# Performance work log

Hardware: AMD Instinct MI355X
Metric: run time of the kernel (lower is better)

## Reference

```python
import jax, jax.numpy as jnp
import numpy as np

B, S, D = 4, 2048, 2048


def setup_inputs() -> dict:
    key = jax.random.key(0)
    ks = jax.random.split(key, 24)
    sc = 1.0 / np.sqrt(D)
    def lin(ki, kb):
        W = jax.random.normal(ks[ki], (D, D), dtype=jnp.float32) * sc
        b = jax.random.normal(ks[kb], (D,), dtype=jnp.float32) * 0.01
        return W, b
    Wi, bWi = lin(0, 1); Ui, bUi = lin(2, 3)
    Wf, bWf = lin(4, 5); Uf, bUf = lin(6, 7)
    Wc, bWc = lin(8, 9); Uc, bUc = lin(10, 11)
    Wo, bWo = lin(12, 13); Uo, bUo = lin(14, 15)
    Wp, bp = lin(16, 17)
    x = jax.random.normal(ks[18], (B, S, D), dtype=jnp.float32)
    h = jax.random.normal(ks[19], (B, S, D), dtype=jnp.float32)
    return dict(x=x, h=h, Wi=Wi, bWi=bWi, Ui=Ui, bUi=bUi,
                Wf=Wf, bWf=bWf, Uf=Uf, bUf=bUf,
                Wc=Wc, bWc=bWc, Uc=Uc, bUc=bUc,
                Wo=Wo, bWo=bWo, Uo=Uo, bUo=bUo,
                Wp=Wp, bp=bp)


def reference(x, h, Wi, bWi, Ui, bUi, Wf, bWf, Uf, bUf,
              Wc, bWc, Uc, bUc, Wo, bWo, Uo, bUo, Wp, bp):
    # In the torch source, h[:, t, :] is read BEFORE being overwritten at step t,
    # and c is zero-initialized with each slot written once (so f * c_prev == 0).
    # Hence the computation is exactly parallel over the time axis.
    Zi = jnp.einsum('bsd,ed->bse', x, Wi) + bWi + jnp.einsum('bsd,ed->bse', h, Ui) + bUi
    Zf = jnp.einsum('bsd,ed->bse', x, Wf) + bWf + jnp.einsum('bsd,ed->bse', h, Uf) + bUf
    Zc = jnp.einsum('bsd,ed->bse', x, Wc) + bWc + jnp.einsum('bsd,ed->bse', h, Uc) + bUc
    Zo = jnp.einsum('bsd,ed->bse', x, Wo) + bWo + jnp.einsum('bsd,ed->bse', h, Uo) + bUo
    i = jnp.exp(Zi)
    f = jnp.exp(Zf)  # multiplies a zero cell state in the source; kept for fidelity
    c = f * jnp.zeros_like(f) + i * jnp.tanh(Zc)
    h_out = jax.nn.sigmoid(Zo) * jnp.tanh(c)
    hidden_state = h_out[:, -1, :] @ Wp.T + bp
    return (hidden_state, c)
```

## Files before the change

kernel.cpp:

```cpp
#include <hip/hip_runtime.h>
#include <hip/hip_bf16.h>

typedef short short8 __attribute__((ext_vector_type(8)));
typedef unsigned short ushort8v __attribute__((ext_vector_type(8)));
typedef float f32x4 __attribute__((ext_vector_type(4)));

#define D_DIM 2048
#define KTOT 4096
#define M_TOT 8192
#define NPACK 4096


__device__ __forceinline__ unsigned short f2bf(float f) {
    union { float f; unsigned u; } c; c.f = f;
    unsigned u = c.u;
    u += 0x7fffu + ((u >> 16) & 1u);
    return (unsigned short)(u >> 16);
}

__device__ __forceinline__ float fast_tanh(float x) {
    float ax = fabsf(x);
    float ez = __expf(2.0f * fminf(ax, 15.0f));
    float t = (ez - 1.0f) / (ez + 1.0f);
    return copysignf(t, x);
}

#define GLOAD_LDS16(g, l)                                                     \
    __builtin_amdgcn_global_load_lds(                                         \
        (const __attribute__((address_space(1))) void*)(g),                   \
        (__attribute__((address_space(3))) void*)(l), 16, 0, 0)


__global__ __launch_bounds__(256)
void pack2(const float* __restrict__ X, const float* __restrict__ H,
           __hip_bfloat16* __restrict__ dst, int total8) {
    int t = blockIdx.x * 256 + threadIdx.x;
    if (t >= total8) return;
    long e0 = (long)t * 8;
    long r  = e0 >> 12;
    int  k  = (int)(e0 & 4095);
    const float* src = (k < D_DIM) ? (X + r * D_DIM + k)
                                   : (H + r * D_DIM + (k - D_DIM));
    float4 v0 = *(const float4*)(src);
    float4 v1 = *(const float4*)(src + 4);
    ushort8v o;
    o[0] = f2bf(v0.x); o[1] = f2bf(v0.y); o[2] = f2bf(v0.z); o[3] = f2bf(v0.w);
    o[4] = f2bf(v1.x); o[5] = f2bf(v1.y); o[6] = f2bf(v1.z); o[7] = f2bf(v1.w);
    *(ushort8v*)(dst + e0) = o;
}


__global__ __launch_bounds__(256)
void pack_gates(const float* __restrict__ Wi, const float* __restrict__ Ui,
                const float* __restrict__ Wc, const float* __restrict__ Uc,
                __hip_bfloat16* __restrict__ dst) {
    int t = blockIdx.x * 256 + threadIdx.x;
    const int g = t >> 9;
    const int k = (t & 511) * 8;
    const int w = g & 31;
    const int n = ((g >> 5) << 4) | (w & 15);
    const float* Wm = (w & 16) ? Wc : Wi;
    const float* Um = (w & 16) ? Uc : Ui;
    const float* src = (k < D_DIM) ? (Wm + (size_t)n * D_DIM + k)
                                   : (Um + (size_t)n * D_DIM + (k - D_DIM));
    float4 v0 = *(const float4*)(src);
    float4 v1 = *(const float4*)(src + 4);
    ushort8v o;
    o[0] = f2bf(v0.x); o[1] = f2bf(v0.y); o[2] = f2bf(v0.z); o[3] = f2bf(v0.w);
    o[4] = f2bf(v1.x); o[5] = f2bf(v1.y); o[6] = f2bf(v1.z); o[7] = f2bf(v1.w);
    *(ushort8v*)(dst + (size_t)g * KTOT + k) = o;
}


#define BK 64
#define NT (KTOT / BK)

__device__ __forceinline__ void stage_half(const __hip_bfloat16* __restrict__ mat,
                                           __hip_bfloat16* ldsHalf,
                                           int rowbase, int kcol0,
                                           int wid, int lane) {
    #pragma unroll
    for (int j = 0; j < 2; ++j) {
        const int Lb  = wid * 128 + j * 64;
        const int L   = Lb + lane;
        const int row = L >> 2;
        const int ul  = (L & 3) ^ ((L >> 3) & 3);
        const __hip_bfloat16* src =
            mat + (size_t)(rowbase + row) * KTOT + kcol0 + ul * 8;
        GLOAD_LDS16(src, (char*)ldsHalf + Lb * 16);
    }
}

__global__ __launch_bounds__(512, 2)
void gemm8(const __hip_bfloat16* __restrict__ A,
           const __hip_bfloat16* __restrict__ Bp,
           const float* __restrict__ bWi, const float* __restrict__ bUi,
           const float* __restrict__ bWc, const float* __restrict__ bUc,
           float* __restrict__ Cout) {
    __shared__ __hip_bfloat16 sA[2][2][256][32];
    __shared__ __hip_bfloat16 sB[2][2][256][32];

    const int tid  = threadIdx.x;
    const int wid  = tid >> 6;
    const int lane = tid & 63;

    int bid = blockIdx.x;
    bid = (bid & 7) * 64 + (bid >> 3);
    const int tn = (bid & 15) * 256;
    const int tm = (bid >> 4) * 256;

    const int wr  = (wid >> 2) * 128;
    const int wc  = (wid & 3) * 64;
    const int r15 = lane & 15;
    const int uswz16 = (((lane >> 4) ^ ((r15 >> 1) & 3)) * 16);

    f32x4 acc[8][4] = {};

    stage_half(A,  &sA[0][0][0][0], tm, 0,  wid, lane);
    stage_half(Bp, &sB[0][0][0][0], tn, 0,  wid, lane);
    stage_half(A,  &sA[0][1][0][0], tm, 32, wid, lane);
    stage_half(Bp, &sB[0][1][0][0], tn, 32, wid, lane);
    asm volatile("s_waitcnt vmcnt(4)" ::: "memory");
    __builtin_amdgcn_s_barrier();

    short8 af[4], bf[4];

    for (int t = 0; t < NT; ++t) {
        const int cur = t & 1, nxt = cur ^ 1;
        const bool pf = (t + 1 < NT);
        const int kc1 = (t + 1) * BK;
        const char* pA = (const char*)sA[cur];
        const char* pB = (const char*)sB[cur];

        #pragma unroll
        for (int m = 0; m < 4; ++m)
            af[m] = *(const short8*)(pA + (size_t)(wr + m * 16 + r15) * 64 + uswz16);
        #pragma unroll
        for (int n = 0; n < 4; ++n)
            bf[n] = *(const short8*)(pB + (size_t)(wc + n * 16 + r15) * 64 + uswz16);
        if (pf) stage_half(A, &sA[nxt][0][0][0], tm, kc1, wid, lane);
        __builtin_amdgcn_s_barrier();
        asm volatile("s_waitcnt lgkmcnt(0)" ::: "memory");
        __builtin_amdgcn_s_setprio(1);
        #pragma unroll
        for (int m = 0; m < 4; ++m)
            #pragma unroll
            for (int n = 0; n < 4; ++n)
                acc[m][n] = __builtin_amdgcn_mfma_f32_16x16x32_bf16(
                    af[m], bf[n], acc[m][n], 0, 0, 0);
        __builtin_amdgcn_s_setprio(0);
        __builtin_amdgcn_s_barrier();

        #pragma unroll
        for (int m = 0; m < 4; ++m)
            af[m] = *(const short8*)(pA + (size_t)(wr + 64 + m * 16 + r15) * 64 + uswz16);
        if (pf) stage_half(Bp, &sB[nxt][0][0][0], tn, kc1, wid, lane);
        __builtin_amdgcn_s_barrier();
        asm volatile("s_waitcnt lgkmcnt(0)" ::: "memory");
        __builtin_amdgcn_s_setprio(1);
        #pragma unroll
        for (int m = 0; m < 4; ++m)
            #pragma unroll
            for (int n = 0; n < 4; ++n)
                acc[4 + m][n] = __builtin_amdgcn_mfma_f32_16x16x32_bf16(
                    af[m], bf[n], acc[4 + m][n], 0, 0, 0);
        __builtin_amdgcn_s_setprio(0);
        if (t < NT - 1) asm volatile("s_waitcnt vmcnt(4)" ::: "memory");
        else            asm volatile("s_waitcnt vmcnt(0)" ::: "memory");
        __builtin_amdgcn_s_barrier();

        #pragma unroll
        for (int m = 0; m < 4; ++m)
            af[m] = *(const short8*)(pA + 16384 + (size_t)(wr + m * 16 + r15) * 64 + uswz16);
        #pragma unroll
        for (int n = 0; n < 4; ++n)
            bf[n] = *(const short8*)(pB + 16384 + (size_t)(wc + n * 16 + r15) * 64 + uswz16);
        if (pf) stage_half(A, &sA[nxt][1][0][0], tm, kc1 + 32, wid, lane);
        __builtin_amdgcn_s_barrier();
        asm volatile("s_waitcnt lgkmcnt(0)" ::: "memory");
        __builtin_amdgcn_s_setprio(1);
        #pragma unroll
        for (int m = 0; m < 4; ++m)
            #pragma unroll
            for (int n = 0; n < 4; ++n)
                acc[m][n] = __builtin_amdgcn_mfma_f32_16x16x32_bf16(
                    af[m], bf[n], acc[m][n], 0, 0, 0);
        __builtin_amdgcn_s_setprio(0);
        __builtin_amdgcn_s_barrier();

        #pragma unroll
        for (int m = 0; m < 4; ++m)
            af[m] = *(const short8*)(pA + 16384 + (size_t)(wr + 64 + m * 16 + r15) * 64 + uswz16);
        if (pf) stage_half(Bp, &sB[nxt][1][0][0], tn, kc1 + 32, wid, lane);
        __builtin_amdgcn_s_barrier();
        asm volatile("s_waitcnt lgkmcnt(0)" ::: "memory");
        __builtin_amdgcn_s_setprio(1);
        #pragma unroll
        for (int m = 0; m < 4; ++m)
            #pragma unroll
            for (int n = 0; n < 4; ++n)
                acc[4 + m][n] = __builtin_amdgcn_mfma_f32_16x16x32_bf16(
                    af[m], bf[n], acc[4 + m][n], 0, 0, 0);
        __builtin_amdgcn_s_setprio(0);
        asm volatile("s_waitcnt vmcnt(4)" ::: "memory");
        __builtin_amdgcn_s_barrier();
    }

    const int rg4 = (lane >> 4) * 4;
    #pragma unroll
    for (int q = 0; q < 2; ++q) {
        const int gn = (tn >> 1) + (wc >> 1) + q * 16 + r15;
        const float bi_ = bWi[gn] + bUi[gn];
        const float bc_ = bWc[gn] + bUc[gn];
        #pragma unroll
        for (int m = 0; m < 8; ++m) {
            const int gm = tm + wr + m * 16 + rg4;
            #pragma unroll
            for (int r = 0; r < 4; ++r) {
                const float zi = acc[m][2 * q][r]     + bi_;
                const float zc = acc[m][2 * q + 1][r] + bc_;
                Cout[(size_t)(gm + r) * D_DIM + gn] = __expf(zi) * fast_tanh(zc);
            }
        }
    }
}


__global__ __launch_bounds__(256)
void last_gate(const float* __restrict__ x, const float* __restrict__ h,
               const float* __restrict__ Wo, const float* __restrict__ bWo,
               const float* __restrict__ Uo, const float* __restrict__ bUo,
               const float* __restrict__ cfull, float* __restrict__ hbuf) {
    const int o    = blockIdx.x * 4 + (threadIdx.x >> 6);
    const int lane = threadIdx.x & 63;
    const int b = o >> 11, e = o & 2047;
    const float* xr = x  + ((size_t)b * D_DIM + (D_DIM - 1)) * D_DIM;
    const float* hr = h  + ((size_t)b * D_DIM + (D_DIM - 1)) * D_DIM;
    const float* wo = Wo + (size_t)e * D_DIM;
    const float* uo = Uo + (size_t)e * D_DIM;
    float s = 0.0f;
    for (int d = lane; d < D_DIM; d += 64)
        s += xr[d] * wo[d] + hr[d] * uo[d];
    #pragma unroll
    for (int off = 32; off; off >>= 1) s += __shfl_down(s, off);
    if (lane == 0) {
        const float zo  = s + bWo[e] + bUo[e];
        const float sig = 1.0f / (1.0f + __expf(-zo));
        const float cv  = cfull[((size_t)b * D_DIM + (D_DIM - 1)) * D_DIM + e];
        hbuf[o] = sig * fast_tanh(cv);
    }
}


__global__ __launch_bounds__(256)
void proj(const float* __restrict__ hbuf, const float* __restrict__ Wp,
          const float* __restrict__ bp, float* __restrict__ out) {
    const int o    = blockIdx.x * 4 + (threadIdx.x >> 6);
    const int lane = threadIdx.x & 63;
    const int b = o >> 11, p = o & 2047;
    const float* hv = hbuf + (size_t)b * D_DIM;
    const float* wp = Wp   + (size_t)p * D_DIM;
    float s = 0.0f;
    for (int e = lane; e < D_DIM; e += 64)
        s += hv[e] * wp[e];
    #pragma unroll
    for (int off = 32; off; off >>= 1) s += __shfl_down(s, off);
    if (lane == 0) out[o] = s + bp[p];
}


extern "C" void kernel_launch(void* const* d_in, const int* in_sizes, int n_in,
                              void* d_out, int out_size, void* d_ws, size_t ws_size,
                              hipStream_t stream) {
    const float* x   = (const float*)d_in[0];
    const float* h   = (const float*)d_in[1];
    const float* Wi  = (const float*)d_in[2];  const float* bWi = (const float*)d_in[3];
    const float* Ui  = (const float*)d_in[4];  const float* bUi = (const float*)d_in[5];
    const float* Wc  = (const float*)d_in[10]; const float* bWc = (const float*)d_in[11];
    const float* Uc  = (const float*)d_in[12]; const float* bUc = (const float*)d_in[13];
    const float* Wo  = (const float*)d_in[14]; const float* bWo = (const float*)d_in[15];
    const float* Uo  = (const float*)d_in[16]; const float* bUo = (const float*)d_in[17];
    const float* Wp  = (const float*)d_in[18]; const float* bp  = (const float*)d_in[19];

    float* out = (float*)d_out;
    char*  ws  = (char*)d_ws;

    __hip_bfloat16* Abf  = (__hip_bfloat16*)ws;
    __hip_bfloat16* Bpk  = (__hip_bfloat16*)(ws + ((size_t)64 << 20));
    float*          hbuf = (float*)(ws + ((size_t)96 << 20));

    pack2<<<16384, 256, 0, stream>>>(x, h, Abf, M_TOT * KTOT / 8);
    pack_gates<<<8192, 256, 0, stream>>>(Wi, Ui, Wc, Uc, Bpk);

    gemm8<<<(M_TOT / 256) * (NPACK / 256), 512, 0, stream>>>(
        Abf, Bpk, bWi, bUi, bWc, bUc, out + 8192);

    last_gate<<<2048, 256, 0, stream>>>(x, h, Wo, bWo, Uo, bUo, out + 8192,
                                        (float*)hbuf);
    proj<<<2048, 256, 0, stream>>>(hbuf, Wp, bp, out);
}
```

Before: 374.2 us.

## Double-buffer MFMA fragments in registers and overlap LDS reads with compute

After: 334.6 us. -10.6%, faster.

```diff
diff --git a/kernel.cpp b/kernel.cpp
--- a/kernel.cpp
+++ b/kernel.cpp
@@ -91,6 +91,23 @@
     }
 }
 
+__device__ __forceinline__ void read4(short8 (&dst)[4], const char* base,
+                                      int roff, int uswz16) {
+    #pragma unroll
+    for (int m = 0; m < 4; ++m)
+        dst[m] = *(const short8*)(base + (size_t)(roff + m * 16) * 64 + uswz16);
+}
+
+__device__ __forceinline__ void mfma16(f32x4 (&acc)[8][4], int mb,
+                                       const short8 (&a)[4], const short8 (&b)[4]) {
+    #pragma unroll
+    for (int m = 0; m < 4; ++m)
+        #pragma unroll
+        for (int n = 0; n < 4; ++n)
+            acc[mb + m][n] = __builtin_amdgcn_mfma_f32_16x16x32_bf16(
+                a[m], b[n], acc[mb + m][n], 0, 0, 0);
+}
+
 __global__ __launch_bounds__(512, 2)
 void gemm8(const __hip_bfloat16* __restrict__ A,
            const __hip_bfloat16* __restrict__ Bp,
@@ -114,7 +131,11 @@
     const int r15 = lane & 15;
     const int uswz16 = (((lane >> 4) ^ ((r15 >> 1) & 3)) * 16);
 
+    const int rA  = wr + r15;
+    const int rB  = wc + r15;
+
     f32x4 acc[8][4] = {};
+    short8 aP[4], aQ[4], bP[4], bQ[4];
 
     stage_half(A,  &sA[0][0][0][0], tm, 0,  wid, lane);
     stage_half(Bp, &sB[0][0][0][0], tn, 0,  wid, lane);
@@ -122,88 +143,69 @@
     stage_half(Bp, &sB[0][1][0][0], tn, 32, wid, lane);
     asm volatile("s_waitcnt vmcnt(4)" ::: "memory");
     __builtin_amdgcn_s_barrier();
-
-    short8 af[4], bf[4];
+    read4(aP, (const char*)&sA[0][0][0][0], rA, uswz16);
+    read4(bP, (const char*)&sB[0][0][0][0], rB, uswz16);
 
     for (int t = 0; t < NT; ++t) {
         const int cur = t & 1, nxt = cur ^ 1;
         const bool pf = (t + 1 < NT);
         const int kc1 = (t + 1) * BK;
-        const char* pA = (const char*)sA[cur];
-        const char* pB = (const char*)sB[cur];
-
-        #pragma unroll
-        for (int m = 0; m < 4; ++m)
-            af[m] = *(const short8*)(pA + (size_t)(wr + m * 16 + r15) * 64 + uswz16);
-        #pragma unroll
-        for (int n = 0; n < 4; ++n)
-            bf[n] = *(const short8*)(pB + (size_t)(wc + n * 16 + r15) * 64 + uswz16);
-        if (pf) stage_half(A, &sA[nxt][0][0][0], tm, kc1, wid, lane);
+        const char* cA0 = (const char*)&sA[cur][0][0][0];
+        const char* cA1 = (const char*)&sA[cur][1][0][0];
+        const char* cB1 = (const char*)&sB[cur][1][0][0];
+        const char* nA0 = (const char*)&sA[nxt][0][0][0];
+        const char* nB0 = (const char*)&sB[nxt][0][0][0];
+
+        read4(aQ, cA0, rA + 64, uswz16);
+        if (pf) {
+            stage_half(A, &sA[nxt][0][0][0], tm, kc1, wid, lane);
+            asm volatile("s_waitcnt vmcnt(2)" ::: "memory");
+        } else {
+            asm volatile("s_waitcnt vmcnt(0)" ::: "memory");
+        }
         __builtin_amdgcn_s_barrier();
-        asm volatile("s_waitcnt lgkmcnt(0)" ::: "memory");
+        asm volatile("s_waitcnt lgkmcnt(4)" ::: "memory");
+        __builtin_amdgcn_sched_barrier(0);
         __builtin_amdgcn_s_setprio(1);
-        #pragma unroll
-        for (int m = 0; m < 4; ++m)
-            #pragma unroll
-            for (int n = 0; n < 4; ++n)
-                acc[m][n] = __builtin_amdgcn_mfma_f32_16x16x32_bf16(
-                    af[m], bf[n], acc[m][n], 0, 0, 0);
+        mfma16(acc, 0, aP, bP);
         __builtin_amdgcn_s_setprio(0);
-        __builtin_amdgcn_s_barrier();
-
-        #pragma unroll
-        for (int m = 0; m < 4; ++m)
-            af[m] = *(const short8*)(pA + (size_t)(wr + 64 + m * 16 + r15) * 64 + uswz16);
+
+        read4(aP, cA1, rA, uswz16);
+        read4(bQ, cB1, rB, uswz16);
         if (pf) stage_half(Bp, &sB[nxt][0][0][0], tn, kc1, wid, lane);
         __builtin_amdgcn_s_barrier();
-        asm volatile("s_waitcnt lgkmcnt(0)" ::: "memory");
+        asm volatile("s_waitcnt lgkmcnt(8)" ::: "memory");
+        __builtin_amdgcn_sched_barrier(0);
         __builtin_amdgcn_s_setprio(1);
-        #pragma unroll
-        for (int m = 0; m < 4; ++m)
-            #pragma unroll
-            for (int n = 0; n < 4; ++n)
-                acc[4 + m][n] = __builtin_amdgcn_mfma_f32_16x16x32_bf16(
-                    af[m], bf[n], acc[4 + m][n], 0, 0, 0);
+        mfma16(acc, 4, aQ, bP);
         __builtin_amdgcn_s_setprio(0);
-        if (t < NT - 1) asm volatile("s_waitcnt vmcnt(4)" ::: "memory");
-        else            asm volatile("s_waitcnt vmcnt(0)" ::: "memory");
+
+        read4(aQ, cA1, rA + 64, uswz16);
+        if (pf) {
+            stage_half(A, &sA[nxt][1][0][0], tm, kc1 + 32, wid, lane);
+            asm volatile("s_waitcnt vmcnt(2)" ::: "memory");
+        } else {
+            asm volatile("s_waitcnt vmcnt(0)" ::: "memory");
+        }
         __builtin_amdgcn_s_barrier();
-
-        #pragma unroll
-        for (int m = 0; m < 4; ++m)
-            af[m] = *(const short8*)(pA + 16384 + (size_t)(wr + m * 16 + r15) * 64 + uswz16);
-        #pragma unroll
-        for (int n = 0; n < 4; ++n)
-            bf[n] = *(const short8*)(pB + 16384 + (size_t)(wc + n * 16 + r15) * 64 + uswz16);
-        if (pf) stage_half(A, &sA[nxt][1][0][0], tm, kc1 + 32, wid, lane);
+        asm volatile("s_waitcnt lgkmcnt(4)" ::: "memory");
+        __builtin_amdgcn_sched_barrier(0);
+        __builtin_amdgcn_s_setprio(1);
+        mfma16(acc, 0, aP, bQ);
+        __builtin_amdgcn_s_setprio(0);
+
+        if (pf) {
+            read4(aP, nA0, rA, uswz16);
+            read4(bP, nB0, rB, uswz16);
+            stage_half(Bp, &sB[nxt][1][0][0], tn, kc1 + 32, wid, lane);
+        }
         __builtin_amdgcn_s_barrier();
-        asm volatile("s_waitcnt lgkmcnt(0)" ::: "memory");
+        if (pf) asm volatile("s_waitcnt lgkmcnt(8)" ::: "memory");
+        else    asm volatile("s_waitcnt lgkmcnt(0)" ::: "memory");
+        __builtin_amdgcn_sched_barrier(0);
         __builtin_amdgcn_s_setprio(1);
-        #pragma unroll
-        for (int m = 0; m < 4; ++m)
-            #pragma unroll
-            for (int n = 0; n < 4; ++n)
-                acc[m][n] = __builtin_amdgcn_mfma_f32_16x16x32_bf16(
-                    af[m], bf[n], acc[m][n], 0, 0, 0);
+        mfma16(acc, 4, aQ, bQ);
         __builtin_amdgcn_s_setprio(0);
-        __builtin_amdgcn_s_barrier();
-
-        #pragma unroll
-        for (int m = 0; m < 4; ++m)
-            af[m] = *(const short8*)(pA + 16384 + (size_t)(wr + 64 + m * 16 + r15) * 64 + uswz16);
-        if (pf) stage_half(Bp, &sB[nxt][1][0][0], tn, kc1 + 32, wid, lane);
-        __builtin_amdgcn_s_barrier();
-        asm volatile("s_waitcnt lgkmcnt(0)" ::: "memory");
-        __builtin_amdgcn_s_setprio(1);
-        #pragma unroll
-        for (int m = 0; m < 4; ++m)
-            #pragma unroll
-            for (int n = 0; n < 4; ++n)
-                acc[4 + m][n] = __builtin_amdgcn_mfma_f32_16x16x32_bf16(
-                    af[m], bf[n], acc[4 + m][n], 0, 0, 0);
-        __builtin_amdgcn_s_setprio(0);
-        asm volatile("s_waitcnt vmcnt(4)" ::: "memory");
-        __builtin_amdgcn_s_barrier();
     }
 
     const int rg4 = (lane >> 4) * 4;
```
